# Performance work log

Measured on AMD Instinct MI355X. Metric: run time of the kernel, lower is better.

## Reference

```python
import jax, jax.numpy as jnp
import numpy as np

# ---- Plane / hashgrid static configuration (matches init_kwargs + gridencoder defaults) ----
LEVEL_DIM = 2
NUM_LEVELS = 16
LOG2_HASHMAP = 19
HASHMAP_MAX = 2 ** LOG2_HASHMAP
BASE_RES = 16               # gridencoder default base_resolution
RESOLUTION = 2048           # desired_resolution
OUTPUT_DIM = 8
HIDDEN_DIM = 64
N_POINTS = 1 << 20
PRIME_Y = np.uint32(2654435761)  # torch-ngp fast_hash prime for dim 1 (dim 0 prime is 1)

# per-level scales / resolutions / table offsets, exactly as in gridencoder
_b = np.exp2(np.log2(RESOLUTION / BASE_RES) / (NUM_LEVELS - 1))
SCALES, RESOLUTIONS, OFFSETS = [], [], [0]
for _l in range(NUM_LEVELS):
    _s = BASE_RES * (_b ** _l) - 1.0
    _r = int(np.ceil(_s)) + 1
    SCALES.append(float(_s)); RESOLUTIONS.append(_r)
    _p = min(HASHMAP_MAX, _r * _r)
    _p = (_p + 7) // 8 * 8  # align to 8 entries
    OFFSETS.append(OFFSETS[-1] + _p)
TOTAL_PARAMS = OFFSETS[-1]


def grid_encode(x, table):
    """Multires 2D hashgrid encoding. x: [N,2] in [0,1], table: [TOTAL_PARAMS, LEVEL_DIM]."""
    feats = []
    for l in range(NUM_LEVELS):
        scale, res = SCALES[l], RESOLUTIONS[l]
        size = OFFSETS[l + 1] - OFFSETS[l]
        pos = x * scale + 0.5                 # [N,2]
        pg = jnp.floor(pos)
        fr = pos - pg                         # bilinear fractions within grid cell
        pg = pg.astype(jnp.uint32)
        acc = jnp.zeros((x.shape[0], LEVEL_DIM), x.dtype)
        for dx in (0, 1):
            for dy in (0, 1):
                gx = pg[:, 0] + jnp.uint32(dx)
                gy = pg[:, 1] + jnp.uint32(dy)
                if res * res > size:
                    # hashed level: fast_hash (xor of prime-multiplied coords) mod table size
                    idx = (gx ^ (gy * PRIME_Y)) % jnp.uint32(size)
                else:
                    # dense level: row-major index, wrapped like the CUDA kernel
                    idx = (gx + gy * jnp.uint32(res)) % jnp.uint32(size)
                wx = fr[:, 0] if dx else 1.0 - fr[:, 0]
                wy = fr[:, 1] if dy else 1.0 - fr[:, 1]
                acc = acc + (wx * wy)[:, None] * table[OFFSETS[l] + idx.astype(jnp.int32)]
        feats.append(acc)
    return jnp.concatenate(feats, axis=-1)  # [N, NUM_LEVELS*LEVEL_DIM] = [N, 32]


def mlp(h, w0, w1):
    # 2-layer bias-free MLP: Linear(32->64) + relu + Linear(64->8)
    return jax.nn.relu(h @ w0.T) @ w1.T


def plane_forward(xy, table, w0, w1, bound):
    xy = (xy + bound) / (2 * bound)
    coords = jnp.clip(xy * RESOLUTION - 0.5, 0, RESOLUTION - 1)
    cx, cy = coords[..., 0], coords[..., 1]
    cx0, cy0 = jnp.floor(cx), jnp.floor(cy)
    cx1 = jnp.clip(cx0 + 1, 0, RESOLUTION - 1)
    cy1 = jnp.clip(cy0 + 1, 0, RESOLUTION - 1)
    u = (cx - cx0)[..., None]
    v = (cy - cy0)[..., None]

    def corner(a, b):
        g = (jnp.stack([a, b], axis=-1) + 0.5) / RESOLUTION
        return mlp(grid_encode(g, table), w0, w1)

    f00 = corner(cx0, cy0)
    f01 = corner(cx0, cy1)
    f10 = corner(cx1, cy0)
    f11 = corner(cx1, cy1)
    return (1 - v) * (1 - u) * f00 + (1 - v) * u * f10 + v * (1 - u) * f01 + v * u * f11


def setup_inputs() -> dict:
    key = jax.random.key(0)
    k1, k2, k3, k4 = jax.random.split(key, 4)
    xy = jax.random.normal(k1, (N_POINTS, 2), jnp.float32)
    table = jax.random.uniform(k2, (TOTAL_PARAMS, LEVEL_DIM), jnp.float32, -1e-4, 1e-4)
    in_dim = NUM_LEVELS * LEVEL_DIM
    w0 = jax.random.normal(k3, (HIDDEN_DIM, in_dim), jnp.float32) * (1.0 / np.sqrt(in_dim))
    w1 = jax.random.normal(k4, (OUTPUT_DIM, HIDDEN_DIM), jnp.float32) * (1.0 / np.sqrt(HIDDEN_DIM))
    return {"xy": xy, "table": table, "w0": w0, "w1": w1, "bound": 1}


def reference(xy, table, w0, w1, bound):
    return plane_forward(xy, table, w0, w1, bound)
```

## Files before the change

### kernel.cpp

```cpp
#include <hip/hip_runtime.h>
#include <math.h>

#define PRIME_Y 2654435761u

struct LevelParams { float scale; unsigned res; unsigned size; unsigned offset; };
struct EncParams { LevelParams lv[16]; };

typedef __attribute__((ext_vector_type(8))) short short8;
typedef __attribute__((ext_vector_type(4))) float f32x4;

struct alignas(8) F2 { float x, y; };

__device__ inline unsigned bf2pack(float a, float b) {
  unsigned r;
  asm("v_cvt_pk_bf16_f32 %0, %1, %2" : "=v"(r) : "v"(a), "v"(b));
  return r;
}
__device__ inline F2 bf2unpack(unsigned u) {
  F2 r;
  r.x = __uint_as_float(u << 16);
  r.y = __uint_as_float(u & 0xFFFF0000u);
  return r;
}

__global__ __launch_bounds__(256) void cvt_table(const F2* __restrict__ in,
                                                 unsigned* __restrict__ outb,
                                                 int n) {
  int i = blockIdx.x * 256 + threadIdx.x;
  if (i < n) {
    F2 v = in[i];
    outb[i] = bf2pack(v.x, v.y);
  }
}

__global__ __launch_bounds__(256) void prep3(
    const F2* __restrict__ in, uint4* __restrict__ quad,
    unsigned* __restrict__ hp, EncParams P, unsigned denseTotal,
    unsigned total) {
  unsigned i = blockIdx.x * 256 + threadIdx.x;
  if (i >= total) return;
  if (i >= denseTotal) {
    F2 a = in[i];
    hp[i - denseTotal] = bf2pack(a.x, a.y);
    return;
  }
  unsigned off = 0, size = 0, res = 0;
  #pragma unroll
  for (int l = 0; l < 12; ++l)
    if (i >= P.lv[l].offset) {
      off = P.lv[l].offset; size = P.lv[l].size; res = P.lv[l].res;
    }
  unsigned j = i - off;
  unsigned j1 = j + 1u;        if (j1 >= size) j1 -= size;
  unsigned j2 = j + res;       if (j2 >= size) j2 -= size;
  unsigned j3 = j + res + 1u;  if (j3 >= size) j3 -= size;
  F2 a0 = in[off + j],  a1 = in[off + j1];
  F2 a2 = in[off + j2], a3 = in[off + j3];
  quad[i] = make_uint4(bf2pack(a0.x, a0.y), bf2pack(a1.x, a1.y),
                       bf2pack(a2.x, a2.y), bf2pack(a3.x, a3.y));
}

#define SMEM_BYTES 27648
#define SMEM_FB 39936

__global__ __launch_bounds__(256, 4) void plane_fwd1(
    const F2* __restrict__ xy,
    const uint4* __restrict__ qtab,
    const unsigned* __restrict__ hp,
    const float* __restrict__ w0g,
    const float* __restrict__ w1g,
    const int* __restrict__ boundp,
    float* __restrict__ out,
    EncParams P)
{
  __shared__ __align__(16) char smem[SMEM_BYTES];
  const int t = threadIdx.x;
  const int L = t & 63;
  const int w = t >> 6;
  const int r16 = L & 15;
  const int g = L >> 4;
  const int role = L & 1;

  {
    const float4* s = (const float4*)w0g;
    float4 a = s[t * 2], b = s[t * 2 + 1];
    uint4 pk = make_uint4(bf2pack(a.x, a.y), bf2pack(a.z, a.w),
                          bf2pack(b.x, b.y), bf2pack(b.z, b.w));
    *(uint4*)(smem + (t >> 2) * 80 + (t & 3) * 16) = pk;
  }
  {
    int row = t >> 4;
    int colb = (t & 15) * 8;
    float c0 = 0.f, c1 = 0.f, c2 = 0.f, c3 = 0.f;
    if (row < 8) {
      float4 wv = *(const float4*)(w1g + row * 64 + (t & 15) * 4);
      c0 = wv.x; c1 = wv.y; c2 = wv.z; c3 = wv.w;
    }
    *(uint2*)(smem + 5120 + row * 128 + (colb ^ ((row & 7) << 4))) =
        make_uint2(bf2pack(c0, c1), bf2pack(c2, c3));
  }

  char* sFH = smem + 7168 + w * 5120;

  const int pt = blockIdx.x * 128 + w * 32 + (L >> 1);
  F2 pxy = xy[pt];

  int braw = boundp[0];
  float bf = (braw > 0x00800000) ? __int_as_float(braw) : (float)braw;
  float inv2b = 0.5f / bf;
  float xn = (pxy.x + bf) * inv2b;
  float yn = (pxy.y + bf) * inv2b;

  float cx  = fminf(fmaxf(xn * 2048.0f - 0.5f, 0.0f), 2047.0f);
  float cyv = fminf(fmaxf(yn * 2048.0f - 0.5f, 0.0f), 2047.0f);
  float cx0 = floorf(cx), cy0 = floorf(cyv);
  float u = cx - cx0, v = cyv - cy0;
  float cx1 = fminf(cx0 + 1.0f, 2047.0f);
  float cy1 = fminf(cy0 + 1.0f, 2047.0f);

  const float K = 1.0f / 2048.0f;
  const float gxc0 = (cx0 + 0.5f) * K, gxc1 = (cx1 + 0.5f) * K;
  const float gyc0 = (cy0 + 0.5f) * K, gyc1 = (cy1 + 0.5f) * K;
  const float gy = role ? gyc1 : gyc0;

  const unsigned denseOff = P.lv[12].offset;
  unsigned fw2[2][16];

  #pragma unroll
  for (int li = 0; li < 4; ++li) {
    const int l = 12 + li;
    const float scale   = P.lv[l].scale;
    const unsigned size = P.lv[l].size;
    const unsigned off  = P.lv[l].offset;
    const unsigned m = size - 1u;
    const unsigned* tb = hp + (off - denseOff);

    float px0 = fmaf(gxc0, scale, 0.5f), px1 = fmaf(gxc1, scale, 0.5f);
    float py  = fmaf(gy,   scale, 0.5f);
    float fx0 = floorf(px0), fx1 = floorf(px1), fyv = floorf(py);
    unsigned ux0 = (unsigned)fx0, ux1 = (unsigned)fx1;
    unsigned uy  = (unsigned)fyv;
    bool xs = (ux1 != ux0);

    unsigned hya = uy * PRIME_Y;
    unsigned hyb = hya + PRIME_Y;

    unsigned h00 = tb[(ux0 ^ hya) & m];
    unsigned h10 = tb[((ux0 + 1u) ^ hya) & m];
    unsigned h01 = tb[(ux0 ^ hyb) & m];
    unsigned h11 = tb[((ux0 + 1u) ^ hyb) & m];
    unsigned h20 = 0u, h21 = 0u;
    if (xs) { h20 = tb[((ux0 + 2u) ^ hya) & m];
              h21 = tb[((ux0 + 2u) ^ hyb) & m]; }

    float frx0 = px0 - fx0, frx1 = px1 - fx1;
    float fry = py - fyv;

    #pragma unroll
    for (int c = 0; c < 2; ++c) {
      bool sx = (c != 0) && xs;
      unsigned e00 = sx ? h10 : h00;
      unsigned e10 = sx ? h20 : h10;
      unsigned e01 = sx ? h11 : h01;
      unsigned e11 = sx ? h21 : h11;
      float frx = c ? frx1 : frx0;
      F2 t00 = bf2unpack(e00), t10 = bf2unpack(e10);
      F2 t01 = bf2unpack(e01), t11 = bf2unpack(e11);
      float wx0 = 1.0f - frx, wx1 = frx;
      float wy0 = 1.0f - fry, wy1 = fry;
      float w00 = wx0 * wy0, w01 = wx0 * wy1;
      float w10 = wx1 * wy0, w11 = wx1 * wy1;
      float fx = w00 * t00.x + w01 * t01.x + w10 * t10.x + w11 * t11.x;
      float fy = w00 * t00.y + w01 * t01.y + w10 * t10.y + w11 * t11.y;
      fw2[c][l] = bf2pack(fx, fy);
    }
  }

  #pragma unroll
  for (int l = 0; l < 12; ++l) {
    const float scale   = P.lv[l].scale;
    const unsigned res  = P.lv[l].res;
    const unsigned off  = P.lv[l].offset;
    const uint4* qt = qtab + off;

    float px0 = fmaf(gxc0, scale, 0.5f), px1 = fmaf(gxc1, scale, 0.5f);
    float py  = fmaf(gy,   scale, 0.5f);
    float fx0 = floorf(px0), fx1 = floorf(px1), fyv = floorf(py);
    unsigned ux0 = (unsigned)fx0, ux1 = (unsigned)fx1;
    unsigned uy  = (unsigned)fyv;
    bool xs = (ux1 != ux0);

    unsigned vA = ux0 + uy * res;
    uint4 qA = qt[vA];
    uint4 qB = make_uint4(0u, 0u, 0u, 0u);
    if (xs) qB = qt[vA + 1u];

    float frx0 = px0 - fx0, frx1 = px1 - fx1;
    float fry = py - fyv;

    #pragma unroll
    for (int c = 0; c < 2; ++c) {
      bool sx = (c != 0) && xs;
      unsigned qx = sx ? qB.x : qA.x;
      unsigned qy = sx ? qB.y : qA.y;
      unsigned qz = sx ? qB.z : qA.z;
      unsigned qw = sx ? qB.w : qA.w;
      float frx = c ? frx1 : frx0;
      F2 t00 = bf2unpack(qx), t10 = bf2unpack(qy);
      F2 t01 = bf2unpack(qz), t11 = bf2unpack(qw);
      float wx0 = 1.0f - frx, wx1 = frx;
      float wy0 = 1.0f - fry, wy1 = fry;
      float w00 = wx0 * wy0, w01 = wx0 * wy1;
      float w10 = wx1 * wy0, w11 = wx1 * wy1;
      float fx = w00 * t00.x + w01 * t01.x + w10 * t10.x + w11 * t11.x;
      float fy = w00 * t00.y + w01 * t01.y + w10 * t10.y + w11 * t11.y;
      fw2[c][l] = bf2pack(fx, fy);
    }
  }

  __syncthreads();

  f32x4 outacc[4];
  #pragma unroll
  for (int b = 0; b < 4; ++b) outacc[b] = (f32x4){0.f, 0.f, 0.f, 0.f};

  #pragma unroll
  for (int rr = 0; rr < 2; ++rr) {
    *(uint4*)(sFH + L * 80 +  0) =
        make_uint4(fw2[rr][0],  fw2[rr][1],  fw2[rr][2],  fw2[rr][3]);
    *(uint4*)(sFH + L * 80 + 16) =
        make_uint4(fw2[rr][4],  fw2[rr][5],  fw2[rr][6],  fw2[rr][7]);
    *(uint4*)(sFH + L * 80 + 32) =
        make_uint4(fw2[rr][8],  fw2[rr][9],  fw2[rr][10], fw2[rr][11]);
    *(uint4*)(sFH + L * 80 + 48) =
        make_uint4(fw2[rr][12], fw2[rr][13], fw2[rr][14], fw2[rr][15]);

    short8 bfr[4];
    #pragma unroll
    for (int b = 0; b < 4; ++b)
      bfr[b] = *(const short8*)(sFH + (16 * b + r16) * 80 + g * 16);

    f32x4 oacc[4];
    #pragma unroll
    for (int b = 0; b < 4; ++b) oacc[b] = (f32x4){0.f, 0.f, 0.f, 0.f};

    #pragma unroll
    for (int h = 0; h < 2; ++h) {
      #pragma unroll
      for (int ai = 0; ai < 2; ++ai) {
        const int a = 2 * h + ai;
        short8 afr = *(const short8*)(smem + (16 * a + r16) * 80 + g * 16);
        f32x4 acc[4];
        #pragma unroll
        for (int b = 0; b < 4; ++b) acc[b] = (f32x4){0.f, 0.f, 0.f, 0.f};
        #pragma unroll
        for (int b = 0; b < 4; ++b)
          acc[b] = __builtin_amdgcn_mfma_f32_16x16x32_bf16(afr, bfr[b],
                                                           acc[b], 0, 0, 0);
        #pragma unroll
        for (int b = 0; b < 4; ++b) {
          f32x4 hh = acc[b];
          float h0 = fmaxf(hh.x, 0.f), h1 = fmaxf(hh.y, 0.f);
          float h2 = fmaxf(hh.z, 0.f), h3 = fmaxf(hh.w, 0.f);
          const int row = 16 * b + r16;
          *(uint2*)(sFH + row * 64 +
                    ((ai * 32 + g * 8) ^ ((row & 3) << 4))) =
              make_uint2(bf2pack(h0, h1), bf2pack(h2, h3));
        }
      }
      short8 a2 = *(const short8*)(smem + 5120 + r16 * 128 +
                                   ((h * 64 + g * 16) ^ ((r16 & 7) << 4)));
      #pragma unroll
      for (int b = 0; b < 4; ++b) {
        const int row = 16 * b + r16;
        short8 b2 = *(const short8*)(sFH + row * 64 +
                                     ((g * 16) ^ ((row & 3) << 4)));
        oacc[b] = __builtin_amdgcn_mfma_f32_16x16x32_bf16(a2, b2, oacc[b],
                                                          0, 0, 0);
      }
    }

    float wcr = (rr ? u : 1.0f - u) * (role ? v : 1.0f - v);
    #pragma unroll
    for (int b = 0; b < 4; ++b) {
      float wcm = __shfl(wcr, 16 * b + r16, 64);
      outacc[b].x = fmaf(wcm, oacc[b].x, outacc[b].x);
      outacc[b].y = fmaf(wcm, oacc[b].y, outacc[b].y);
      outacc[b].z = fmaf(wcm, oacc[b].z, outacc[b].z);
      outacc[b].w = fmaf(wcm, oacc[b].w, outacc[b].w);
    }
  }

  #pragma unroll
  for (int b = 0; b < 4; ++b) {
    outacc[b].x += __shfl_xor(outacc[b].x, 1, 64);
    outacc[b].y += __shfl_xor(outacc[b].y, 1, 64);
    outacc[b].z += __shfl_xor(outacc[b].z, 1, 64);
    outacc[b].w += __shfl_xor(outacc[b].w, 1, 64);
  }
  if ((r16 & 1) == 0 && g < 2) {
    #pragma unroll
    for (int b = 0; b < 4; ++b) {
      int po = blockIdx.x * 128 + w * 32 + ((16 * b + r16) >> 1);
      *(f32x4*)(out + (size_t)po * 8 + 4 * g) = outacc[b];
    }
  }
}

template <int TBF>
__global__ __launch_bounds__(256, 4) void plane_fwd(
    const F2* __restrict__ xy,
    const F2* __restrict__ table,
    const unsigned* __restrict__ tbf16,
    const float* __restrict__ w0g,
    const float* __restrict__ w1g,
    const int* __restrict__ boundp,
    float* __restrict__ out,
    EncParams P)
{
  __shared__ __align__(16) char smem[SMEM_FB];
  const int t = threadIdx.x;
  const int L = t & 63;
  const int w = t >> 6;
  const int r16 = L & 15;
  const int g = L >> 4;

  {
    const float4* s = (const float4*)w0g;
    float4 a = s[t * 2], b = s[t * 2 + 1];
    uint4 pk = make_uint4(bf2pack(a.x, a.y), bf2pack(a.z, a.w),
                          bf2pack(b.x, b.y), bf2pack(b.z, b.w));
    *(uint4*)(smem + (t >> 2) * 80 + (t & 3) * 16) = pk;
  }
  {
    int row = t >> 4;
    int colb = (t & 15) * 8;
    float c0 = 0.f, c1 = 0.f, c2 = 0.f, c3 = 0.f;
    if (row < 8) {
      float4 wv = *(const float4*)(w1g + row * 64 + (t & 15) * 4);
      c0 = wv.x; c1 = wv.y; c2 = wv.z; c3 = wv.w;
    }
    *(uint2*)(smem + 5120 + row * 128 + (colb ^ ((row & 7) << 4))) =
        make_uint2(bf2pack(c0, c1), bf2pack(c2, c3));
  }

  char* sFH = smem + 7168 + w * 8192;

  const int gid = blockIdx.x * 256 + t;
  const int p = gid >> 2;
  const int c = t & 3;
  F2 pxy = xy[p];

  int braw = boundp[0];
  float bf = (braw > 0x00800000) ? __int_as_float(braw) : (float)braw;
  float inv2b = 0.5f / bf;
  float xn = (pxy.x + bf) * inv2b;
  float yn = (pxy.y + bf) * inv2b;

  float cx  = fminf(fmaxf(xn * 2048.0f - 0.5f, 0.0f), 2047.0f);
  float cyv = fminf(fmaxf(yn * 2048.0f - 0.5f, 0.0f), 2047.0f);
  float cx0 = floorf(cx), cy0 = floorf(cyv);
  float u = cx - cx0, v = cyv - cy0;
  float cx1 = fminf(cx0 + 1.0f, 2047.0f);
  float cy1 = fminf(cy0 + 1.0f, 2047.0f);

  const float cxc = (c & 1) ? cx1 : cx0;
  const float cyc = (c & 2) ? cy1 : cy0;
  const float wc = ((c & 1) ? u : 1.0f - u) * ((c & 2) ? v : 1.0f - v);

  const float K = 1.0f / 2048.0f;
  const float gx = (cxc + 0.5f) * K;
  const float gy = (cyc + 0.5f) * K;

  unsigned fw[16];

  #pragma unroll
  for (int lidx = 0; lidx < 16; ++lidx) {
    const int l = (lidx < 4) ? (12 + lidx) : (lidx - 4);
    const float scale   = P.lv[l].scale;
    const unsigned res  = P.lv[l].res;
    const unsigned size = P.lv[l].size;
    const unsigned off  = P.lv[l].offset;
    const bool hashed = (res * res) > size;

    float px = fmaf(gx, scale, 0.5f);
    float pgx = floorf(px);
    float frx = px - pgx;
    unsigned ux = (unsigned)pgx;

    float py = fmaf(gy, scale, 0.5f);
    float pgy = floorf(py);
    float fry = py - pgy;
    unsigned uy = (unsigned)pgy;

    unsigned i00, i01, i10, i11;
    if (hashed) {
      const unsigned m = size - 1u;
      unsigned hy0 = uy * PRIME_Y;
      unsigned hy1 = hy0 + PRIME_Y;
      i00 = (ux ^ hy0) & m;
      i01 = (ux ^ hy1) & m;
      i10 = ((ux + 1u) ^ hy0) & m;
      i11 = ((ux + 1u) ^ hy1) & m;
    } else {
      unsigned b0 = uy * res, b1 = b0 + res;
      unsigned q00 = ux + b0,      q01 = ux + b1;
      unsigned q10 = ux + 1u + b0, q11 = ux + 1u + b1;
      i00 = q00 >= size ? q00 - size : q00;
      i01 = q01 >= size ? q01 - size : q01;
      i10 = q10 >= size ? q10 - size : q10;
      i11 = q11 >= size ? q11 - size : q11;
    }

    F2 t00, t01, t10, t11;
    if (TBF == 1) {
      const unsigned* tb = tbf16 + off;
      t00 = bf2unpack(tb[i00]);
      t01 = bf2unpack(tb[i01]);
      t10 = bf2unpack(tb[i10]);
      t11 = bf2unpack(tb[i11]);
    } else {
      const F2* tabp = table + off;
      t00 = tabp[i00]; t01 = tabp[i01]; t10 = tabp[i10]; t11 = tabp[i11];
    }

    float wx0 = 1.0f - frx, wx1 = frx;
    float wy0 = 1.0f - fry, wy1 = fry;
    float w00 = wx0 * wy0, w01 = wx0 * wy1, w10 = wx1 * wy0, w11 = wx1 * wy1;
    float fx = w00 * t00.x + w01 * t01.x + w10 * t10.x + w11 * t11.x;
    float fy = w00 * t00.y + w01 * t01.y + w10 * t10.y + w11 * t11.y;
    fw[l] = bf2pack(fx, fy);
  }

  *(uint4*)(sFH + L * 80 +  0) = make_uint4(fw[0],  fw[1],  fw[2],  fw[3]);
  *(uint4*)(sFH + L * 80 + 16) = make_uint4(fw[4],  fw[5],  fw[6],  fw[7]);
  *(uint4*)(sFH + L * 80 + 32) = make_uint4(fw[8],  fw[9],  fw[10], fw[11]);
  *(uint4*)(sFH + L * 80 + 48) = make_uint4(fw[12], fw[13], fw[14], fw[15]);

  __syncthreads();

  short8 afr[4], bfr[4];
  #pragma unroll
  for (int b = 0; b < 4; ++b)
    bfr[b] = *(const short8*)(sFH + (16 * b + r16) * 80 + g * 16);
  #pragma unroll
  for (int a = 0; a < 4; ++a)
    afr[a] = *(const short8*)(smem + (16 * a + r16) * 80 + g * 16);

  f32x4 acc[4][4];
  #pragma unroll
  for (int a = 0; a < 4; ++a)
    #pragma unroll
    for (int b = 0; b < 4; ++b)
      acc[a][b] = (f32x4){0.f, 0.f, 0.f, 0.f};

  #pragma unroll
  for (int a = 0; a < 4; ++a)
    #pragma unroll
    for (int b = 0; b < 4; ++b)
      acc[a][b] = __builtin_amdgcn_mfma_f32_16x16x32_bf16(
          afr[a], bfr[b], acc[a][b], 0, 0, 0);

  #pragma unroll
  for (int a = 0; a < 4; ++a)
    #pragma unroll
    for (int b = 0; b < 4; ++b) {
      f32x4 h = acc[a][b];
      float h0 = fmaxf(h.x, 0.f), h1 = fmaxf(h.y, 0.f);
      float h2 = fmaxf(h.z, 0.f), h3 = fmaxf(h.w, 0.f);
      *(uint2*)(sFH + (16 * b + r16) * 128 +
                ((a * 32 + g * 8) ^ ((r16 & 7) << 4))) =
          make_uint2(bf2pack(h0, h1), bf2pack(h2, h3));
    }

  f32x4 oacc[4];
  #pragma unroll
  for (int b = 0; b < 4; ++b) oacc[b] = (f32x4){0.f, 0.f, 0.f, 0.f};

  #pragma unroll
  for (int ks = 0; ks < 2; ++ks) {
    short8 a2 = *(const short8*)(smem + 5120 + r16 * 128 +
                                 ((ks * 64 + g * 16) ^ ((r16 & 7) << 4)));
    #pragma unroll
    for (int b = 0; b < 4; ++b) {
      short8 b2 = *(const short8*)(sFH + (16 * b + r16) * 128 +
                                   ((ks * 64 + g * 16) ^ ((r16 & 7) << 4)));
      oacc[b] = __builtin_amdgcn_mfma_f32_16x16x32_bf16(a2, b2, oacc[b], 0, 0, 0);
    }
  }

  #pragma unroll
  for (int b = 0; b < 4; ++b) {
    float wcm = __shfl(wc, 16 * b + r16, 64);
    float v0 = oacc[b].x * wcm;
    float v1 = oacc[b].y * wcm;
    float v2 = oacc[b].z * wcm;
    float v3 = oacc[b].w * wcm;
    v0 += __shfl_xor(v0, 1, 64); v0 += __shfl_xor(v0, 2, 64);
    v1 += __shfl_xor(v1, 1, 64); v1 += __shfl_xor(v1, 2, 64);
    v2 += __shfl_xor(v2, 1, 64); v2 += __shfl_xor(v2, 2, 64);
    v3 += __shfl_xor(v3, 1, 64); v3 += __shfl_xor(v3, 2, 64);
    if ((L & 3) == 0 && g < 2) {
      int pt = blockIdx.x * 64 + w * 16 + 4 * b + (r16 >> 2);
      *(f32x4*)(out + (size_t)pt * 8 + 4 * g) = (f32x4){v0, v1, v2, v3};
    }
  }
}

extern "C" void kernel_launch(void* const* d_in, const int* in_sizes, int n_in,
                              void* d_out, int out_size, void* d_ws, size_t ws_size,
                              hipStream_t stream) {
  EncParams P;
  double b = exp2(log2(2048.0 / 16.0) / 15.0);
  unsigned off = 0;
  for (int l = 0; l < 16; ++l) {
    double s = 16.0 * pow(b, (double)l) - 1.0;
    int r = (int)ceil(s) + 1;
    unsigned p = (unsigned)(r * r);
    if (p > 524288u) p = 524288u;
    p = (p + 7u) / 8u * 8u;
    P.lv[l].scale = (float)s;
    P.lv[l].res = (unsigned)r;
    P.lv[l].size = p;
    P.lv[l].offset = off;
    off += p;
  }
  const int total_params = (int)off;

  int hstart = 16;
  for (int l = 0; l < 16; ++l) {
    unsigned long long rr = (unsigned long long)P.lv[l].res * P.lv[l].res;
    if (rr > P.lv[l].size) { hstart = l; break; }
  }
  const unsigned denseTotal = (hstart < 16) ? P.lv[hstart].offset
                                            : (unsigned)total_params;
  const size_t quadBytes = (size_t)denseTotal * 16;
  const size_t hashBytes = (size_t)((unsigned)total_params - denseTotal) * 4;
  const size_t packBytes = (size_t)total_params * 4;

  const int N = in_sizes[0] / 2;
  const F2* xy = (const F2*)d_in[0];
  const F2* table = (const F2*)d_in[1];
  const float* w0g = (const float*)d_in[2];
  const float* w1g = (const float*)d_in[3];
  const int* bp = (const int*)d_in[4];
  float* outp = (float*)d_out;

  if (hstart == 12 && (N & 127) == 0 && ws_size >= quadBytes + hashBytes) {
    uint4* quad = (uint4*)d_ws;
    unsigned* hp = (unsigned*)((char*)d_ws + quadBytes);
    prep3<<<(total_params + 255) / 256, 256, 0, stream>>>(
        table, quad, hp, P, denseTotal, (unsigned)total_params);
    plane_fwd1<<<N / 128, 256, 0, stream>>>(xy, quad, hp, w0g, w1g, bp,
                                            outp, P);
  } else if (ws_size >= packBytes) {
    unsigned* tbf = (unsigned*)d_ws;
    cvt_table<<<(total_params + 255) / 256, 256, 0, stream>>>(table, tbf,
                                                              total_params);
    plane_fwd<1><<<N / 64, 256, 0, stream>>>(xy, table, tbf, w0g, w1g, bp,
                                             outp, P);
  } else {
    plane_fwd<0><<<N / 64, 256, 0, stream>>>(xy, table, nullptr, w0g, w1g, bp,
                                             outp, P);
  }
}
```

Before: 268.1 us.

## Share hashed-level corner rows between paired lanes via shuffles; pad hidden smem rows

For the four hashed levels, each lane of a pair now loads only its own y row of table entries. When the two y corners share the same grid row, the partner lane fetches the extra row above, and the results are exchanged with __shfl_xor. This cuts the redundant global gathers that both lanes previously issued, at the cost of extra shuffles and selects. Separately, the hidden-activation LDS buffer swaps its XOR swizzle for a padded row stride of 80. That removes index arithmetic but may change bank conflicts and requires the buffer to be large enough for the wider stride.

```diff
diff --git a/kernel.cpp b/kernel.cpp
--- a/kernel.cpp
+++ b/kernel.cpp
@@ -136,34 +136,49 @@
     const unsigned* tb = hp + (off - denseOff);
 
     float px0 = fmaf(gxc0, scale, 0.5f), px1 = fmaf(gxc1, scale, 0.5f);
-    float py  = fmaf(gy,   scale, 0.5f);
-    float fx0 = floorf(px0), fx1 = floorf(px1), fyv = floorf(py);
+    float py0 = fmaf(gyc0, scale, 0.5f), py1 = fmaf(gyc1, scale, 0.5f);
+    float fx0 = floorf(px0), fx1 = floorf(px1);
+    float fy0 = floorf(py0), fy1 = floorf(py1);
     unsigned ux0 = (unsigned)fx0, ux1 = (unsigned)fx1;
-    unsigned uy  = (unsigned)fyv;
-    bool xs = (ux1 != ux0);
-
-    unsigned hya = uy * PRIME_Y;
-    unsigned hyb = hya + PRIME_Y;
-
-    unsigned h00 = tb[(ux0 ^ hya) & m];
-    unsigned h10 = tb[((ux0 + 1u) ^ hya) & m];
-    unsigned h01 = tb[(ux0 ^ hyb) & m];
-    unsigned h11 = tb[((ux0 + 1u) ^ hyb) & m];
-    unsigned h20 = 0u, h21 = 0u;
-    if (xs) { h20 = tb[((ux0 + 2u) ^ hya) & m];
-              h21 = tb[((ux0 + 2u) ^ hyb) & m]; }
-
-    float frx0 = px0 - fx0, frx1 = px1 - fx1;
-    float fry = py - fyv;
+    unsigned uyB = (unsigned)fy0, uy1 = (unsigned)fy1;
+    bool xs = (ux1 != ux0), ys = (uy1 != uyB);
+
+    unsigned hB = uyB * PRIME_Y;
+    unsigned hOwn = hB + (role ? PRIME_Y : 0u);
+    unsigned o0 = tb[(ux0 ^ hOwn) & m];
+    unsigned o1 = tb[((ux0 + 1u) ^ hOwn) & m];
+    unsigned o2 = 0u;
+    if (xs) o2 = tb[((ux0 + 2u) ^ hOwn) & m];
+    unsigned x0 = 0u, x1 = 0u, x2 = 0u;
+    if (!role && ys) {
+      unsigned hX = hB + 2u * PRIME_Y;
+      x0 = tb[(ux0 ^ hX) & m];
+      x1 = tb[((ux0 + 1u) ^ hX) & m];
+      if (xs) x2 = tb[((ux0 + 2u) ^ hX) & m];
+    }
+    bool sendX = (!role) && ys;
+    unsigned s0 = sendX ? x0 : o0;
+    unsigned s1 = sendX ? x1 : o1;
+    unsigned s2 = sendX ? x2 : o2;
+    unsigned r0 = __shfl_xor(s0, 1, 64);
+    unsigned r1 = __shfl_xor(s1, 1, 64);
+    unsigned r2 = __shfl_xor(s2, 1, 64);
+    bool swapR = role && !ys;
+    unsigned lo0 = swapR ? r0 : o0, hi0 = swapR ? o0 : r0;
+    unsigned lo1 = swapR ? r1 : o1, hi1 = swapR ? o1 : r1;
+    unsigned lo2 = swapR ? r2 : o2, hi2 = swapR ? o2 : r2;
+
+    float fry = role ? (py1 - fy1) : (py0 - fy0);
+    float frx0v = px0 - fx0, frx1v = px1 - fx1;
 
     #pragma unroll
     for (int c = 0; c < 2; ++c) {
       bool sx = (c != 0) && xs;
-      unsigned e00 = sx ? h10 : h00;
-      unsigned e10 = sx ? h20 : h10;
-      unsigned e01 = sx ? h11 : h01;
-      unsigned e11 = sx ? h21 : h11;
-      float frx = c ? frx1 : frx0;
+      unsigned e00 = sx ? lo1 : lo0;
+      unsigned e10 = sx ? lo2 : lo1;
+      unsigned e01 = sx ? hi1 : hi0;
+      unsigned e11 = sx ? hi2 : hi1;
+      float frx = c ? frx1v : frx0v;
       F2 t00 = bf2unpack(e00), t10 = bf2unpack(e10);
       F2 t01 = bf2unpack(e01), t11 = bf2unpack(e11);
       float wx0 = 1.0f - frx, wx1 = frx;
@@ -263,8 +278,7 @@
           float h0 = fmaxf(hh.x, 0.f), h1 = fmaxf(hh.y, 0.f);
           float h2 = fmaxf(hh.z, 0.f), h3 = fmaxf(hh.w, 0.f);
           const int row = 16 * b + r16;
-          *(uint2*)(sFH + row * 64 +
-                    ((ai * 32 + g * 8) ^ ((row & 3) << 4))) =
+          *(uint2*)(sFH + row * 80 + ai * 32 + g * 8) =
               make_uint2(bf2pack(h0, h1), bf2pack(h2, h3));
         }
       }
@@ -273,8 +287,7 @@
       #pragma unroll
       for (int b = 0; b < 4; ++b) {
         const int row = 16 * b + r16;
-        short8 b2 = *(const short8*)(sFH + row * 64 +
-                                     ((g * 16) ^ ((row & 3) << 4)));
+        short8 b2 = *(const short8*)(sFH + row * 80 + g * 16);
         oacc[b] = __builtin_amdgcn_mfma_f32_16x16x32_bf16(a2, b2, oacc[b],
                                                           0, 0, 0);
       }
```

Result: faster. 249.1 us (-7.1%).
